# Performance work log

Hardware: AMD Instinct MI355X
Metric: run time of the kernel (lower is better)

The kernel has to match this reference:

```python
import jax, jax.numpy as jnp
import numpy as np

B, FIN, N, T = 16, 3, 170, 288   # batch, input features, vertices, timesteps
H, O, K, KS = 64, 64, 3, 3       # hidden, out features, Chebyshev order, temporal kernel


def _build_adj_and_cheb(n, k, seed=0):
    rng = np.random.default_rng(seed)
    A = rng.random((n, n)).astype(np.float32)
    A = (A + A.T) / 2.0
    np.fill_diagonal(A, 0.0)
    d = A.sum(axis=1)
    L = np.diag(d) - A
    d_inv_sqrt = np.where(d > 0, d ** -0.5, 0.0).astype(np.float32)
    L_norm = d_inv_sqrt[:, None] * L * d_inv_sqrt[None, :]
    lam_max = float(np.max(np.linalg.eigvals(L_norm).real))
    L_scaled = (2.0 / lam_max) * L_norm - np.eye(n, dtype=np.float32)
    polys = [np.eye(n, dtype=np.float32), L_scaled]
    for _ in range(2, k):
        polys.append(2.0 * L_scaled @ polys[-1] - polys[-2])
    return A, np.stack(polys[:k]).astype(np.float32)


def setup_inputs() -> dict:
    key = jax.random.key(0)
    ks = jax.random.split(key, 6)
    A, cheb = _build_adj_and_cheb(N, K)
    return {
        "x": jax.random.normal(ks[0], (B, FIN, N, T), jnp.float32),
        "adj": jnp.asarray(A),
        "cheb": jnp.asarray(cheb),                                   # [K,N,N]
        "conv_w": jax.random.normal(ks[1], (H, FIN, 1, KS), jnp.float32) * 0.1,
        "conv_b": jax.random.normal(ks[2], (H,), jnp.float32) * 0.1,
        "theta": jax.random.normal(ks[3], (K, H, O), jnp.float32) * 0.05,
        "res_w": jax.random.normal(ks[4], (O, FIN), jnp.float32) * 0.1,
        "res_b": jax.random.normal(ks[5], (O,), jnp.float32) * 0.1,
    }


def reference(x, adj, cheb, conv_w, conv_b, theta, res_w, res_b):
    # x: [B, FIN, N, T]; adj is unused by forward (cheb polys are precomputed)
    pad = KS // 2
    # TemporalConvLayer: Conv2d(FIN->H, kernel (1,KS), pad (0,KS//2)) + ReLU
    t = jax.lax.conv_general_dilated(
        x, conv_w, window_strides=(1, 1), padding=((0, 0), (pad, pad)),
        dimension_numbers=("NCHW", "OIHW", "NCHW"))
    t = jax.nn.relu(t + conv_b[None, :, None, None])        # [B,H,N,T]
    t = jnp.transpose(t, (0, 3, 2, 1))                      # [B,T,N,H]
    # ChebConv: sum_k (T_k @ x_t) @ Theta_k, fused over time and K, then ReLU
    z = jnp.einsum("knm,btmc->kbtnc", cheb, t)              # [K,B,T,N,H]
    gcn = jax.nn.relu(jnp.einsum("kbtnc,kco->btno", z, theta))  # [B,T,N,O]
    # residual Linear(FIN -> O) applied to x permuted to [B,T,N,FIN]
    res = jnp.einsum("bfnt,of->btno", x, res_w) + res_b     # [B,T,N,O]
    out = gcn + res
    return jnp.transpose(out, (0, 3, 2, 1))                 # [B,O,N,T]
```

## Files before the change

kernel.cpp:

```cpp
#include <hip/hip_runtime.h>
#include <hip/hip_bf16.h>


#define Bx   16
#define FINx 3
#define Nx   170
#define Tx   288
#define Hx   64
#define Ox   64
#define Kx   3
#define NP   192
#define XSW  10
#define NBT  (Bx * Tx)
#define TPAD 36

#define CHEBF_ELEMS (Kx * 6 * 12 * 64 * 8)
#define THF_ELEMS   (Kx * 2 * 4 * 64 * 8)
#define WF_ELEMS    (4 * 64 * 8)
#define TMP_ELEMS   ((size_t)NBT * Ox * NP)
#define TMP_BYTES   (TMP_ELEMS * 2)

typedef __attribute__((ext_vector_type(8))) short bf16x8;
typedef __attribute__((ext_vector_type(4))) short bf16x4;
typedef __attribute__((ext_vector_type(4))) float f32x4;
typedef __attribute__((ext_vector_type(8))) short short8;

__device__ __align__(16) __hip_bfloat16 g_chebfrag[CHEBF_ELEMS];
__device__ __align__(16) __hip_bfloat16 g_thfrag[THF_ELEMS];
__device__ __align__(16) __hip_bfloat16 g_wfrag[WF_ELEMS];
__device__ __align__(16) __hip_bfloat16 g_tmp[TMP_ELEMS];

static __device__ __forceinline__ short f2bf(float f) {
    __hip_bfloat16 h = __float2bfloat16(f);
    return *reinterpret_cast<short*>(&h);
}
static __device__ __forceinline__ float bf2f(short s) {
    __hip_bfloat16 h = *reinterpret_cast<__hip_bfloat16*>(&s);
    return __bfloat162float(h);
}

__global__ __launch_bounds__(512)
void precompute_frag(const float* __restrict__ cheb, const float* __restrict__ theta,
                     const float* __restrict__ conv_w, const float* __restrict__ conv_b) {
    int idx = blockIdx.x * 512 + threadIdx.x;
    if (idx < CHEBF_ELEMS) {
        int j = idx & 7, lane = (idx >> 3) & 63, rest = idx >> 9;
        int nt = rest % 12; rest /= 12;
        int s = rest % 6, k = rest / 6;
        int n = nt * 16 + (lane & 15);
        int m = s * 32 + (lane >> 4) * 8 + j;
        float v = (n < Nx && m < Nx) ? cheb[(k * Nx + n) * Nx + m] : 0.f;
        g_chebfrag[idx] = __float2bfloat16(v);
    } else if (idx < CHEBF_ELEMS + THF_ELEMS) {
        int jdx = idx - CHEBF_ELEMS;
        int j = jdx & 7, lane = (jdx >> 3) & 63, rest = jdx >> 9;
        int ot = rest % 4; rest /= 4;
        int s = rest % 2, k = rest / 2;
        int o = ot * 16 + (lane & 15);
        int c = s * 32 + (lane >> 4) * 8 + j;
        g_thfrag[jdx] = __float2bfloat16(theta[(k * Hx + c) * Ox + o]);
    } else if (idx < CHEBF_ELEMS + THF_ELEMS + WF_ELEMS) {
        int jdx = idx - CHEBF_ELEMS - THF_ELEMS;
        int j = jdx & 7, lane = (jdx >> 3) & 63, ct = jdx >> 9;
        int c = ct * 16 + (lane & 15);
        int slot = (lane >> 4) * 8 + j;
        float v = 0.f;
        if (slot < 9) v = conv_w[c * 9 + slot];
        else if (slot == 9) v = conv_b[c];
        g_wfrag[jdx] = __float2bfloat16(v);
    }
}

static __device__ __forceinline__ int stm_off(int m, int byte) {
    return m * 128 + (byte ^ ((m & 7) << 4));
}
static __device__ __forceinline__ int szk_off(int o, int byte) {
    return o * 384 + (byte ^ ((o & 7) << 4));
}

__global__ __launch_bounds__(512, 4)
void stgcn_fused9(const float* __restrict__ x,
                  __hip_bfloat16* __restrict__ tmp) {
    __shared__ __align__(16) char sTm[NP * 128];
    __shared__ __align__(16) char sZk[Ox * 384];
    __shared__ __hip_bfloat16 sXs[NP * XSW];

    const int tid = threadIdx.x;
    const int vid = (blockIdx.x & 7) * 576 + (blockIdx.x >> 3);
    const int b  = vid / Tx;
    const int t0 = vid % Tx;

    for (int idx = tid; idx < NP * XSW; idx += 512) {
        int n = idx / XSW, r = idx % XSW;
        float v = 0.f;
        if (n < Nx && r < 9) {
            int f = r / 3, j = r % 3;
            int tt = t0 - 1 + j;
            if (tt >= 0 && tt < Tx) v = x[((b * FINx + f) * Nx + n) * Tx + tt];
        }
        sXs[idx] = __float2bfloat16(v);
    }

    const int lane = tid & 63;
    const int w    = tid >> 6;
    const int l16  = lane & 15;
    const int lk   = lane >> 4;

    const int mg = w & 3;
    const int og = w >> 2;
    const int wr = w & 1;
    const int wc = w >> 1;

    __syncthreads();

    {
        bf16x8 wfr[2], xfr[3];
#pragma unroll
        for (int u = 0; u < 2; ++u)
            wfr[u] = *(const bf16x8*)(&g_wfrag[((og * 2 + u) * 64 + lane) * 8]);
#pragma unroll
        for (int j = 0; j < 3; ++j) {
            int m = (mg * 3 + j) * 16 + l16;
            bf16x8 xf;
#pragma unroll
            for (int q = 0; q < 8; ++q) xf[q] = 0;
            if (lk == 0) {
#pragma unroll
                for (int q = 0; q < 8; ++q)
                    xf[q] = *reinterpret_cast<const short*>(&sXs[m * XSW + q]);
            } else if (lk == 1) {
                xf[0] = *reinterpret_cast<const short*>(&sXs[m * XSW + 8]);
                xf[1] = f2bf(1.0f);
            }
            xfr[j] = xf;
        }
#pragma unroll
        for (int j = 0; j < 3; ++j)
#pragma unroll
            for (int u = 0; u < 2; ++u) {
                f32x4 tacc = (f32x4)0.f;
                tacc = __builtin_amdgcn_mfma_f32_16x16x32_bf16(wfr[u], xfr[j], tacc, 0, 0, 0);
                int m  = (mg * 3 + j) * 16 + l16;
                int c0 = (og * 2 + u) * 16 + lk * 4;
                bf16x4 v;
#pragma unroll
                for (int r = 0; r < 4; ++r) v[r] = f2bf(fmaxf(tacc[r], 0.f));
                *(bf16x4*)(sTm + stm_off(m, c0 * 2)) = v;
            }
    }
    __syncthreads();

    f32x4 accb[2][3];
#pragma unroll
    for (int oi = 0; oi < 2; ++oi)
#pragma unroll
        for (int nj = 0; nj < 3; ++nj) accb[oi][nj] = (f32x4)0.f;

#pragma unroll
    for (int s = 0; s < 2; ++s) {
        bf16x8 tf[2], nf[3];
#pragma unroll
        for (int oi = 0; oi < 2; ++oi)
            tf[oi] = *(const bf16x8*)(&g_thfrag[((s * 4 + wr * 2 + oi) * 64 + lane) * 8]);
#pragma unroll
        for (int nj = 0; nj < 3; ++nj) {
            int n = (wc * 3 + nj) * 16 + l16;
            nf[nj] = *(const bf16x8*)(sTm + stm_off(n, s * 64 + lk * 16));
        }
#pragma unroll
        for (int oi = 0; oi < 2; ++oi)
#pragma unroll
            for (int nj = 0; nj < 3; ++nj)
                accb[oi][nj] = __builtin_amdgcn_mfma_f32_16x16x32_bf16(tf[oi], nf[nj], accb[oi][nj], 0, 0, 0);
    }

    for (int k = 1; k < Kx; ++k) {
        __syncthreads();

        f32x4 accs[3][2];
#pragma unroll
        for (int j = 0; j < 3; ++j)
#pragma unroll
            for (int u = 0; u < 2; ++u) accs[j][u] = (f32x4)0.f;

#pragma unroll
        for (int s = 0; s < 2; ++s) {
            bf16x8 afr[3], bfr[2];
#pragma unroll
            for (int j = 0; j < 3; ++j) {
                int m = (mg * 3 + j) * 16 + l16;
                afr[j] = *(const bf16x8*)(sTm + stm_off(m, s * 64 + lk * 16));
            }
#pragma unroll
            for (int u = 0; u < 2; ++u)
                bfr[u] = *(const bf16x8*)(&g_thfrag[
                         ((((k * 2 + s) * 4) + og * 2 + u) * 64 + lane) * 8]);
#pragma unroll
            for (int j = 0; j < 3; ++j)
#pragma unroll
                for (int u = 0; u < 2; ++u)
                    accs[j][u] = __builtin_amdgcn_mfma_f32_16x16x32_bf16(afr[j], bfr[u], accs[j][u], 0, 0, 0);
        }
#pragma unroll
        for (int j = 0; j < 3; ++j)
#pragma unroll
            for (int u = 0; u < 2; ++u) {
                int o  = (og * 2 + u) * 16 + l16;
                int m0 = (mg * 3 + j) * 16 + lk * 4;
                bf16x4 v;
#pragma unroll
                for (int r = 0; r < 4; ++r) v[r] = f2bf(accs[j][u][r]);
                *(bf16x4*)(sZk + szk_off(o, m0 * 2)) = v;
            }
        __syncthreads();

#pragma unroll
        for (int s = 0; s < 6; ++s) {
            bf16x8 afr2[2], bfr2[3];
#pragma unroll
            for (int oi = 0; oi < 2; ++oi) {
                int o = (wr * 2 + oi) * 16 + l16;
                afr2[oi] = *(const bf16x8*)(sZk + szk_off(o, s * 64 + lk * 16));
            }
#pragma unroll
            for (int nj = 0; nj < 3; ++nj)
                bfr2[nj] = *(const bf16x8*)(&g_chebfrag[
                           ((((k * 6 + s) * 12) + wc * 3 + nj) * 64 + lane) * 8]);
#pragma unroll
            for (int oi = 0; oi < 2; ++oi)
#pragma unroll
                for (int nj = 0; nj < 3; ++nj)
                    accb[oi][nj] = __builtin_amdgcn_mfma_f32_16x16x32_bf16(afr2[oi], bfr2[nj], accb[oi][nj], 0, 0, 0);
        }
    }

    __hip_bfloat16* tbase = tmp + ((size_t)b * Tx + t0) * (Ox * NP);
#pragma unroll
    for (int nj = 0; nj < 3; ++nj) {
        int n = (wc * 3 + nj) * 16 + l16;
#pragma unroll
        for (int oi = 0; oi < 2; ++oi) {
#pragma unroll
            for (int r = 0; r < 4; ++r) {
                int o = (wr * 2 + oi) * 16 + lk * 4 + r;
                tbase[(size_t)o * NP + n] = __float2bfloat16(fmaxf(accb[oi][nj][r], 0.f));
            }
        }
    }
}

__global__ __launch_bounds__(256, 4)
void transpose_res(const __hip_bfloat16* __restrict__ tmp,
                   const float* __restrict__ x,
                   const float* __restrict__ res_w,
                   const float* __restrict__ res_b,
                   float* __restrict__ out) {
    __shared__ float sT[NP * TPAD];

    const int bid = blockIdx.x;
    const int tt  = bid % 9;
    const int o   = (bid / 9) & 63;
    const int b   = bid / (9 * 64);
    const int t0  = tt * 32;
    const int tid = threadIdx.x;

    const float rw0 = res_w[o * 3 + 0], rw1 = res_w[o * 3 + 1], rw2 = res_w[o * 3 + 2];
    const float rb  = res_b[o];

    const __hip_bfloat16* src = tmp + (((size_t)b * Tx + t0) * Ox + o) * NP;
    {
        const int t  = tid >> 3;
        const int n8 = (tid & 7) * 8;
        const __hip_bfloat16* s = src + (size_t)t * (Ox * NP);
#pragma unroll
        for (int i = 0; i < 3; ++i) {
            int n0 = n8 + i * 64;
            short8 v = *(const short8*)(s + n0);
#pragma unroll
            for (int e = 0; e < 8; ++e) {
                int n  = n0 + e;
                int tc = t ^ ((n & 7) * 4);
                sT[n * TPAD + tc] = bf2f(v[e]);
            }
        }
    }
    __syncthreads();
    {
        const int q  = tid & 7;
        const int nr = tid >> 3;
        const float* xb = x + (size_t)(b * FINx) * Nx * Tx + t0 + q * 4;
#pragma unroll
        for (int j = 0; j < 6; ++j) {
            int n = nr + j * 32;
            if (n < Nx) {
                int tc4 = (q ^ (n & 7)) * 4;
                float4 g = *(const float4*)(&sT[n * TPAD + tc4]);
                float4 x0 = *(const float4*)(xb + (size_t)(0 * Nx + n) * Tx);
                float4 x1 = *(const float4*)(xb + (size_t)(1 * Nx + n) * Tx);
                float4 x2 = *(const float4*)(xb + (size_t)(2 * Nx + n) * Tx);
                float4 wv;
                wv.x = g.x + rb + x0.x * rw0 + x1.x * rw1 + x2.x * rw2;
                wv.y = g.y + rb + x0.y * rw0 + x1.y * rw1 + x2.y * rw2;
                wv.z = g.z + rb + x0.z * rw0 + x1.z * rw1 + x2.z * rw2;
                wv.w = g.w + rb + x0.w * rw0 + x1.w * rw1 + x2.w * rw2;
                *(float4*)(&out[((size_t)(b * Ox + o) * Nx + n) * Tx + t0 + q * 4]) = wv;
            }
        }
    }
}

extern "C" void kernel_launch(void* const* d_in, const int* in_sizes, int n_in,
                              void* d_out, int out_size, void* d_ws, size_t ws_size,
                              hipStream_t stream) {
    const float* x      = (const float*)d_in[0];
    const float* cheb   = (const float*)d_in[2];
    const float* conv_w = (const float*)d_in[3];
    const float* conv_b = (const float*)d_in[4];
    const float* theta  = (const float*)d_in[5];
    const float* res_w  = (const float*)d_in[6];
    const float* res_b  = (const float*)d_in[7];
    float* out = (float*)d_out;

    __hip_bfloat16* tmp;
    if (ws_size >= TMP_BYTES) {
        tmp = (__hip_bfloat16*)d_ws;
    } else {
        void* sym = nullptr;
        hipGetSymbolAddress(&sym, HIP_SYMBOL(g_tmp));
        tmp = (__hip_bfloat16*)sym;
    }

    int pre_elems = CHEBF_ELEMS + THF_ELEMS + WF_ELEMS;
    hipLaunchKernelGGL(precompute_frag, dim3((pre_elems + 511) / 512), dim3(512), 0, stream,
                       cheb, theta, conv_w, conv_b);
    hipLaunchKernelGGL(stgcn_fused9, dim3(NBT), dim3(512), 0, stream, x, tmp);
    hipLaunchKernelGGL(transpose_res, dim3(Bx * Ox * 9), dim3(256), 0, stream,
                       tmp, x, res_w, res_b, out);
}
```

Baseline: 159.1 us.

## Double-buffer Z_k in LDS to cut barriers and vectorize tmp stores

Result: slower. 169.1 us (+6.3%).

```diff
diff --git a/kernel.cpp b/kernel.cpp
--- a/kernel.cpp
+++ b/kernel.cpp
@@ -79,10 +79,11 @@
 }
 
 __global__ __launch_bounds__(512, 4)
-void stgcn_fused9(const float* __restrict__ x,
-                  __hip_bfloat16* __restrict__ tmp) {
+void stgcn_fused10(const float* __restrict__ x,
+                   __hip_bfloat16* __restrict__ tmp) {
     __shared__ __align__(16) char sTm[NP * 128];
-    __shared__ __align__(16) char sZk[Ox * 384];
+    __shared__ __align__(16) char sZk1[Ox * 384];
+    __shared__ __align__(16) char sZk2[Ox * 384];
     __shared__ __hip_bfloat16 sXs[NP * XSW];
 
     const int tid = threadIdx.x;
@@ -171,12 +172,13 @@
         for (int oi = 0; oi < 2; ++oi)
 #pragma unroll
             for (int nj = 0; nj < 3; ++nj)
-                accb[oi][nj] = __builtin_amdgcn_mfma_f32_16x16x32_bf16(tf[oi], nf[nj], accb[oi][nj], 0, 0, 0);
-    }
-
+                accb[oi][nj] = __builtin_amdgcn_mfma_f32_16x16x32_bf16(
+                    nf[nj], tf[oi], accb[oi][nj], 0, 0, 0);
+    }
+
+#pragma unroll
     for (int k = 1; k < Kx; ++k) {
-        __syncthreads();
-
+        char* zbuf = (k == 1) ? sZk1 : sZk2;
         f32x4 accs[3][2];
 #pragma unroll
         for (int j = 0; j < 3; ++j)
@@ -199,7 +201,8 @@
             for (int j = 0; j < 3; ++j)
 #pragma unroll
                 for (int u = 0; u < 2; ++u)
-                    accs[j][u] = __builtin_amdgcn_mfma_f32_16x16x32_bf16(afr[j], bfr[u], accs[j][u], 0, 0, 0);
+                    accs[j][u] = __builtin_amdgcn_mfma_f32_16x16x32_bf16(
+                        afr[j], bfr[u], accs[j][u], 0, 0, 0);
         }
 #pragma unroll
         for (int j = 0; j < 3; ++j)
@@ -210,41 +213,47 @@
                 bf16x4 v;
 #pragma unroll
                 for (int r = 0; r < 4; ++r) v[r] = f2bf(accs[j][u][r]);
-                *(bf16x4*)(sZk + szk_off(o, m0 * 2)) = v;
-            }
-        __syncthreads();
-
+                *(bf16x4*)(zbuf + szk_off(o, m0 * 2)) = v;
+            }
+    }
+    __syncthreads();
+
+#pragma unroll
+    for (int k = 1; k < Kx; ++k) {
+        const char* zbuf = (k == 1) ? sZk1 : sZk2;
 #pragma unroll
         for (int s = 0; s < 6; ++s) {
-            bf16x8 afr2[2], bfr2[3];
+            bf16x8 zfr[2], cfr[3];
 #pragma unroll
             for (int oi = 0; oi < 2; ++oi) {
                 int o = (wr * 2 + oi) * 16 + l16;
-                afr2[oi] = *(const bf16x8*)(sZk + szk_off(o, s * 64 + lk * 16));
+                zfr[oi] = *(const bf16x8*)(zbuf + szk_off(o, s * 64 + lk * 16));
             }
 #pragma unroll
             for (int nj = 0; nj < 3; ++nj)
-                bfr2[nj] = *(const bf16x8*)(&g_chebfrag[
-                           ((((k * 6 + s) * 12) + wc * 3 + nj) * 64 + lane) * 8]);
+                cfr[nj] = *(const bf16x8*)(&g_chebfrag[
+                          ((((k * 6 + s) * 12) + wc * 3 + nj) * 64 + lane) * 8]);
 #pragma unroll
             for (int oi = 0; oi < 2; ++oi)
 #pragma unroll
                 for (int nj = 0; nj < 3; ++nj)
-                    accb[oi][nj] = __builtin_amdgcn_mfma_f32_16x16x32_bf16(afr2[oi], bfr2[nj], accb[oi][nj], 0, 0, 0);
+                    accb[oi][nj] = __builtin_amdgcn_mfma_f32_16x16x32_bf16(
+                        cfr[nj], zfr[oi], accb[oi][nj], 0, 0, 0);
         }
     }
 
     __hip_bfloat16* tbase = tmp + ((size_t)b * Tx + t0) * (Ox * NP);
 #pragma unroll
-    for (int nj = 0; nj < 3; ++nj) {
-        int n = (wc * 3 + nj) * 16 + l16;
-#pragma unroll
-        for (int oi = 0; oi < 2; ++oi) {
-#pragma unroll
-            for (int r = 0; r < 4; ++r) {
-                int o = (wr * 2 + oi) * 16 + lk * 4 + r;
-                tbase[(size_t)o * NP + n] = __float2bfloat16(fmaxf(accb[oi][nj][r], 0.f));
-            }
+    for (int oi = 0; oi < 2; ++oi) {
+        int o = (wr * 2 + oi) * 16 + l16;
+#pragma unroll
+        for (int nj = 0; nj < 3; ++nj) {
+            int n0 = (wc * 3 + nj) * 16 + lk * 4;
+            bf16x4 v;
+#pragma unroll
+            for (int r = 0; r < 4; ++r)
+                v[r] = f2bf(fmaxf(accb[oi][nj][r], 0.f));
+            *(bf16x4*)(tbase + (size_t)o * NP + n0) = v;
         }
     }
 }
@@ -333,7 +342,7 @@
     int pre_elems = CHEBF_ELEMS + THF_ELEMS + WF_ELEMS;
     hipLaunchKernelGGL(precompute_frag, dim3((pre_elems + 511) / 512), dim3(512), 0, stream,
                        cheb, theta, conv_w, conv_b);
-    hipLaunchKernelGGL(stgcn_fused9, dim3(NBT), dim3(512), 0, stream, x, tmp);
+    hipLaunchKernelGGL(stgcn_fused10, dim3(NBT), dim3(512), 0, stream, x, tmp);
     hipLaunchKernelGGL(transpose_res, dim3(Bx * Ox * 9), dim3(256), 0, stream,
                        tmp, x, res_w, res_b, out);
 }
```
